# Performance work log

Measured on AMD Instinct MI355X. Metric: run time of the kernel, lower is better.

The kernel has to match this reference:

```python
import jax, jax.numpy as jnp
import numpy as np

B = 16      # number of graphs (equal-sized, batch = repeat(arange(B), N))


def _knn_edges(pos, k, total):
    """Batch-aware kNN graph, torch_geometric knn_graph semantics.

    loop=False, flow='source_to_target': for each query node i, its k nearest
    neighbors j produce edges (row=j neighbor/source, col=i query/target).
    Returns (row, col) as flat global int32 index arrays of length B*N*k.
    """
    N = total // B
    posb = pos.reshape(B, N, -1)                      # [B, N, 3]
    sq = jnp.sum(posb * posb, axis=-1)                # [B, N]
    # squared Euclidean distances, [B, N, N]
    d2 = sq[:, :, None] + sq[:, None, :] - 2.0 * jnp.einsum('bnd,bmd->bnm', posb, posb)
    d2 = jnp.where(jnp.eye(N, dtype=bool)[None], jnp.inf, d2)  # exclude self-loops
    _, nbr = jax.lax.top_k(-d2, k)                    # [B, N, k] local neighbor idx
    offs = (jnp.arange(B, dtype=nbr.dtype) * N)[:, None, None]
    row = (nbr + offs).reshape(-1)                                      # neighbors (sources)
    col = jnp.broadcast_to(jnp.arange(N, dtype=nbr.dtype)[None, :, None] + offs,
                           (B, N, k)).reshape(-1)                       # query nodes (targets)
    return row, col


def reference(x, pos, batch, k):
    total = x.shape[0]
    row, col = _knn_edges(pos, k, total)
    # scatter_mean(x[col], row, dim_size=total): mean of gathered features per row index
    sums = jax.ops.segment_sum(x[col], row, num_segments=total)          # [total, d]
    cnt = jax.ops.segment_sum(jnp.ones(row.shape, x.dtype), row, num_segments=total)
    x_neigh_mean = sums / jnp.maximum(cnt, 1.0)[:, None]                 # empty rows -> 0
    return jnp.sum(jnp.abs(x - x_neigh_mean), axis=-1)                   # L1 norm, [total]


def setup_inputs() -> dict:
    key = jax.random.key(0)
    k1, k2 = jax.random.split(key)
    N = 4096
    x = jax.random.normal(k1, (B * N, 64), dtype=jnp.float32)
    pos = jax.random.normal(k2, (B * N, 3), dtype=jnp.float32)
    batch = jnp.repeat(jnp.arange(B, dtype=jnp.int64), N)
    return {"x": x, "pos": pos, "batch": batch, "k": 10}
```

## Files before the change

kernel.cpp:

```cpp
#include <hip/hip_runtime.h>
#include <stdint.h>

#define NB 16
#define NN 4096
#define KK 10
#define NL 11
#define FD 64
#define TOTAL (NB * NN)
#define NW 8
#define CH 512
#define SOCT 32
#define QG 64
#define WCAP 24
#define WPITCH 25

#define INFF __int_as_float(0x7f800000)

__device__ __forceinline__ float Fd2(float cx, float cy, float cz, float cq,
                                     float vx2, float vy2, float vz2, float sqi) {
    return __fmaf_rn(vz2, cz, __fmaf_rn(vy2, cy, __fmaf_rn(vx2, cx, __fadd_rn(sqi, cq))));
}

__device__ __forceinline__ uint32_t d2exact(float mx, float my, float mz, float sqi,
                                            float cx, float cy, float cz, float cw) {
    float dot = __fadd_rn(__fadd_rn(__fmul_rn(mx, cx), __fmul_rn(my, cy)),
                          __fmul_rn(mz, cz));
    float d2 = __fsub_rn(__fadd_rn(sqi, cw), __fmul_rn(2.0f, dot));
    return __float_as_uint(d2);
}

__global__ __launch_bounds__(256) void prep_kernel(const float* __restrict__ pos,
                                                   float4* __restrict__ pp4,
                                                   int* __restrict__ cnt) {
    const int p = blockIdx.x * 256 + threadIdx.x;
    const float* s = pos + (size_t)p * 6;
    float x0 = s[0], y0 = s[1], z0 = s[2];
    float x1 = s[3], y1 = s[4], z1 = s[5];
    float q0 = __fadd_rn(__fadd_rn(__fmul_rn(x0, x0), __fmul_rn(y0, y0)),
                         __fmul_rn(z0, z0));
    float q1 = __fadd_rn(__fadd_rn(__fmul_rn(x1, x1), __fmul_rn(y1, y1)),
                         __fmul_rn(z1, z1));
    pp4[2 * p + 0] = make_float4(x0, x1, y0, y1);
    pp4[2 * p + 1] = make_float4(z0, z1, q0, q1);
    cnt[2 * p + 0] = 0;
    cnt[2 * p + 1] = 0;
}

__global__ __launch_bounds__(512, 8) void knn_kernel(const float4* __restrict__ pp4,
                                                     int* __restrict__ cnt,
                                                     int* __restrict__ colfix,
                                                     int* __restrict__ nbr) {
    __shared__ uint32_t smem[6400];
    __shared__ float tau_s[QG];
    __shared__ uint32_t qcntw[QG * NW];
    float* listf = (float*)smem;
    uint16_t* pool16 = (uint16_t*)smem;

    const int tid = threadIdx.x;
    const int lane = tid & 63;
    const int w = __builtin_amdgcn_readfirstlane(tid >> 6);
    const int batch = blockIdx.x >> 6;
    const int qloc = ((blockIdx.x & 63) << 6) | lane;
    const int gbase = batch << 12;
    const int gq = gbase + qloc;

    float4 mA = pp4[(gq >> 1) * 2 + 0];
    float4 mB = pp4[(gq >> 1) * 2 + 1];
    const bool hi = (qloc & 1);
    const float mx = hi ? mA.y : mA.x;
    const float my = hi ? mA.w : mA.z;
    const float mz = hi ? mB.y : mB.x;
    const float sqi = hi ? mB.w : mB.z;
    const float vx2 = __fmul_rn(-2.0f, mx);
    const float vy2 = __fmul_rn(-2.0f, my);
    const float vz2 = __fmul_rn(-2.0f, mz);

    const float4* __restrict__ cp = pp4 + (size_t)(gbase + w * CH);

#define D8(cb)                                                        \
    float4 A0 = (cb)[0], B0 = (cb)[1], A1 = (cb)[2], B1 = (cb)[3];    \
    float4 A2 = (cb)[4], B2 = (cb)[5], A3 = (cb)[6], B3 = (cb)[7];    \
    float d0 = Fd2(A0.x, A0.z, B0.x, B0.z, vx2, vy2, vz2, sqi);       \
    float d1 = Fd2(A0.y, A0.w, B0.y, B0.w, vx2, vy2, vz2, sqi);       \
    float d2 = Fd2(A1.x, A1.z, B1.x, B1.z, vx2, vy2, vz2, sqi);       \
    float d3 = Fd2(A1.y, A1.w, B1.y, B1.w, vx2, vy2, vz2, sqi);       \
    float d4 = Fd2(A2.x, A2.z, B2.x, B2.z, vx2, vy2, vz2, sqi);       \
    float d5 = Fd2(A2.y, A2.w, B2.y, B2.w, vx2, vy2, vz2, sqi);       \
    float d6 = Fd2(A3.x, A3.z, B3.x, B3.z, vx2, vy2, vz2, sqi);       \
    float d7 = Fd2(A3.y, A3.w, B3.y, B3.w, vx2, vy2, vz2, sqi);

    float L[NL];
#pragma unroll
    for (int t = 0; t < NL; t++) L[t] = INFF;

#pragma unroll 2
    for (int o = 0; o < SOCT; ++o) {
        const float4* cb = cp + o * 8;
        D8(cb);
        float m = fminf(fminf(fminf(d0, d1), fminf(d2, d3)),
                        fminf(fminf(d4, d5), fminf(d6, d7)));
#pragma unroll
        for (int t = 0; t < NL - 1; ++t) L[t] = __builtin_amdgcn_fmed3f(L[t], L[t + 1], m);
        L[NL - 1] = fminf(L[NL - 1], m);
    }
#pragma unroll
    for (int t = 0; t < NL; t++) listf[tid * NL + t] = L[t];
    __syncthreads();

    if (tid < QG) {
        int p[NW];
#pragma unroll
        for (int u = 0; u < NW; u++) p[u] = NL - 1;
        float tau = INFF;
        for (int it = 0; it < NL; ++it) {
            float best = INFF;
            int bw = 0;
#pragma unroll
            for (int u = 0; u < NW; u++) {
                float v = (p[u] >= 0) ? listf[((u << 6) | tid) * NL + p[u]] : INFF;
                if (v < best) { best = v; bw = u; }
            }
            p[bw]--;
            tau = best;
        }
        tau_s[tid] = tau;
    }
    __syncthreads();

    const float tau = tau_s[lane] * 1.00001f;
    const uint32_t cell0 = (uint32_t)((lane * NW + w) * WPITCH);
    uint32_t cpos = cell0;
    for (int o = 0; o < CH / 8; ++o) {
        const float4* cb = cp + o * 8;
        D8(cb);
        const uint32_t jb = (uint32_t)(w * CH + o * 8);
#define PUSH(dv, off)                                              \
        if ((dv) <= tau && cpos < cell0 + WCAP) {                  \
            pool16[cpos] = (uint16_t)(jb + (off));                 \
            cpos++;                                                \
        }
        PUSH(d0, 0) PUSH(d1, 1) PUSH(d2, 2) PUSH(d3, 3)
        PUSH(d4, 4) PUSH(d5, 5) PUSH(d6, 6) PUSH(d7, 7)
#undef PUSH
    }
    qcntw[lane * NW + w] = cpos - cell0;
    __syncthreads();

    if (tid < QG) {
        uint64_t S[KK];
#pragma unroll
        for (int t = 0; t < KK; t++) S[t] = ~0ull;
#pragma unroll
        for (int u = 0; u < NW; u++) {
            uint32_t c2 = qcntw[tid * NW + u];
            const uint16_t* st = pool16 + (tid * NW + u) * WPITCH;
            for (uint32_t e = 0; e < c2; ++e) {
                uint32_t ix = st[e];
                if (ix == (uint32_t)qloc) continue;
                int g = gbase + (int)ix;
                float4 A = pp4[(g >> 1) * 2 + 0];
                float4 B = pp4[(g >> 1) * 2 + 1];
                bool ch = (ix & 1);
                uint32_t db = d2exact(mx, my, mz, sqi,
                                      ch ? A.y : A.x, ch ? A.w : A.z,
                                      ch ? B.y : B.x, ch ? B.w : B.z);
                uint64_t k64 = ((uint64_t)db << 32) | ix;
                if (k64 < S[0]) {
                    bool sh[KK];
                    sh[0] = true;
#pragma unroll
                    for (int t = 1; t < KK; t++) sh[t] = (k64 < S[t]);
#pragma unroll
                    for (int t = 0; t < KK; t++) {
                        uint64_t vac = sh[t] ? k64 : S[t];
                        S[t] = (t + 1 < KK) ? (sh[t + 1] ? S[t + 1] : vac) : vac;
                    }
                }
            }
        }
#pragma unroll
        for (int t = 0; t < KK; t++) {
            int jl = (int)(S[t] & 0xffffffffu);
            int gj = gbase + jl;
            int p = atomicAdd(&cnt[gj], 1);
            if (colfix) {
                if (p < 64) colfix[(gj << 6) | p] = gq;
            } else {
                nbr[gq * KK + t] = gj;
            }
        }
    }
#undef D8
}

__global__ __launch_bounds__(256) void out_bucket_kernel(const float4* __restrict__ x4,
                                                         const int* __restrict__ colfix,
                                                         const int* __restrict__ cnt,
                                                         float* __restrict__ out) {
    const int gid = blockIdx.x * 256 + threadIdx.x;
    const int n = gid >> 4;
    const int s = gid & 15;
    const int c = cnt[n];
    const int cc = (c > 64) ? 64 : c;
    const int base = n << 6;
    float4 acc = make_float4(0.f, 0.f, 0.f, 0.f);
    int e = 0;
    for (; e + 2 <= cc; e += 2) {
        int q0 = colfix[base + e], q1 = colfix[base + e + 1];
        float4 v0 = x4[(q0 << 4) | s];
        float4 v1 = x4[(q1 << 4) | s];
        acc.x += v0.x; acc.y += v0.y; acc.z += v0.z; acc.w += v0.w;
        acc.x += v1.x; acc.y += v1.y; acc.z += v1.z; acc.w += v1.w;
    }
    if (e < cc) {
        int q0 = colfix[base + e];
        float4 v0 = x4[(q0 << 4) | s];
        acc.x += v0.x; acc.y += v0.y; acc.z += v0.z; acc.w += v0.w;
    }
    const float inv = 1.0f / (float)(c > 1 ? c : 1);
    float4 mn = x4[(n << 4) | s];
    float v = fabsf(mn.x - acc.x * inv) + fabsf(mn.y - acc.y * inv) +
              fabsf(mn.z - acc.z * inv) + fabsf(mn.w - acc.w * inv);
    v += __shfl_xor(v, 1, 64);
    v += __shfl_xor(v, 2, 64);
    v += __shfl_xor(v, 4, 64);
    v += __shfl_xor(v, 8, 64);
    if (s == 0) out[n] = v;
}

__global__ __launch_bounds__(1024) void scan_kernel(const int* __restrict__ cnt,
                                                    int* __restrict__ offs) {
    __shared__ int lds[1024];
    const int t = threadIdx.x;
    const int base = t * 64;
    int s = 0;
    for (int i = 0; i < 64; i++) s += cnt[base + i];
    lds[t] = s;
    __syncthreads();
    for (int off = 1; off < 1024; off <<= 1) {
        int v = (t >= off) ? lds[t - off] : 0;
        __syncthreads();
        lds[t] += v;
        __syncthreads();
    }
    int run = lds[t] - s;
    for (int i = 0; i < 64; i++) {
        offs[base + i] = run;
        run += cnt[base + i];
    }
}

__global__ __launch_bounds__(256) void fill_kernel(const int* __restrict__ nbr,
                                                   int* __restrict__ offs,
                                                   int* __restrict__ col) {
    const int i = blockIdx.x * 256 + threadIdx.x;
#pragma unroll
    for (int t = 0; t < KK; t++) {
        int j = nbr[i * KK + t];
        int p = atomicAdd(&offs[j], 1);
        col[p] = i;
    }
}

__global__ __launch_bounds__(256) void out_kernel(const float* __restrict__ x,
                                                  const int* __restrict__ col,
                                                  const int* __restrict__ offs_end,
                                                  const int* __restrict__ cnt,
                                                  float* __restrict__ out) {
    const int gtid = blockIdx.x * 256 + threadIdx.x;
    const int n = gtid >> 6;
    const int lane = gtid & 63;
    const int c = cnt[n];
    const int end = offs_end[n];
    const int start = end - c;
    float s = 0.0f;
    for (int e = start; e < end; e++) {
        int i = col[e];
        s += x[(size_t)i * FD + lane];
    }
    float mean = s / (float)(c > 1 ? c : 1);
    float v = fabsf(x[(size_t)n * FD + lane] - mean);
#pragma unroll
    for (int off = 32; off; off >>= 1) v += __shfl_xor(v, off, 64);
    if (lane == 0) out[n] = v;
}

extern "C" void kernel_launch(void* const* d_in, const int* in_sizes, int n_in,
                              void* d_out, int out_size, void* d_ws, size_t ws_size,
                              hipStream_t stream) {
    const float* x = (const float*)d_in[0];
    const float* pos = (const float*)d_in[1];
    float* out = (float*)d_out;

    char* ws = (char*)d_ws;
    float4* pp4 = (float4*)(ws + 0);
    int* cnt = (int*)(ws + 1048576);
    int* colfix = (int*)(ws + 1310720);
    int* nbr = (int*)(ws + 1310720);
    int* offs = (int*)(ws + 3932160);
    int* col = (int*)(ws + 4194304);

    const bool bucket = ws_size >= (size_t)(1310720 + TOTAL * 64 * 4);

    hipLaunchKernelGGL(prep_kernel, dim3(TOTAL / 2 / 256), dim3(256), 0, stream, pos, pp4, cnt);
    hipLaunchKernelGGL(knn_kernel, dim3(TOTAL / QG), dim3(512), 0, stream, pp4, cnt,
                       bucket ? colfix : (int*)nullptr, bucket ? (int*)nullptr : nbr);
    if (bucket) {
        hipLaunchKernelGGL(out_bucket_kernel, dim3(TOTAL * 16 / 256), dim3(256), 0, stream,
                           (const float4*)x, colfix, cnt, out);
    } else {
        hipLaunchKernelGGL(scan_kernel, dim3(1), dim3(1024), 0, stream, cnt, offs);
        hipLaunchKernelGGL(fill_kernel, dim3(TOTAL / 256), dim3(256), 0, stream, nbr, offs, col);
        hipLaunchKernelGGL(out_kernel, dim3(TOTAL * FD / 256), dim3(256), 0, stream,
                           x, col, offs, cnt, out);
    }
}
```

Measured before the change: 202.4 us.

## Pack kNN distance math into float2 vectors, interleave batches across blocks, vectorize colfix loads

Distance evaluation in the kNN scan and collection passes now uses two-wide float vectors with fast contraction, so the compiler can emit packed FMA instructions. Block-to-batch mapping is interleaved so consecutive blocks handle different graphs, and the output kernel uses the same interleaving and reads neighbor indices as int4. The collection pass skips the push logic when none of the eight candidates pass, and the threshold slack is widened with an absolute epsilon. The widened slack admits more candidates into the fixed-capacity pools and could overflow them, and the reordered arithmetic may change rounding in the prefilter.

```diff
diff --git a/kernel.cpp b/kernel.cpp
--- a/kernel.cpp
+++ b/kernel.cpp
@@ -16,9 +16,16 @@
 
 #define INFF __int_as_float(0x7f800000)
 
-__device__ __forceinline__ float Fd2(float cx, float cy, float cz, float cq,
-                                     float vx2, float vy2, float vz2, float sqi) {
-    return __fmaf_rn(vz2, cz, __fmaf_rn(vy2, cy, __fmaf_rn(vx2, cx, __fadd_rn(sqi, cq))));
+typedef float f2 __attribute__((ext_vector_type(2)));
+
+__device__ __forceinline__ f2 FdP(f2 cx, f2 cy, f2 cz, f2 cq,
+                                  f2 vx2, f2 vy2, f2 vz2, f2 sqi2) {
+#pragma clang fp contract(fast)
+    f2 t = sqi2 + cq;
+    t = vx2 * cx + t;
+    t = vy2 * cy + t;
+    t = vz2 * cz + t;
+    return t;
 }
 
 __device__ __forceinline__ uint32_t d2exact(float mx, float my, float mz, float sqi,
@@ -59,8 +66,8 @@
     const int tid = threadIdx.x;
     const int lane = tid & 63;
     const int w = __builtin_amdgcn_readfirstlane(tid >> 6);
-    const int batch = blockIdx.x >> 6;
-    const int qloc = ((blockIdx.x & 63) << 6) | lane;
+    const int batch = blockIdx.x & 15;
+    const int qloc = ((blockIdx.x >> 4) << 6) | lane;
     const int gbase = batch << 12;
     const int gq = gbase + qloc;
 
@@ -71,23 +78,22 @@
     const float my = hi ? mA.w : mA.z;
     const float mz = hi ? mB.y : mB.x;
     const float sqi = hi ? mB.w : mB.z;
-    const float vx2 = __fmul_rn(-2.0f, mx);
-    const float vy2 = __fmul_rn(-2.0f, my);
-    const float vz2 = __fmul_rn(-2.0f, mz);
-
-    const float4* __restrict__ cp = pp4 + (size_t)(gbase + w * CH);
-
-#define D8(cb)                                                        \
-    float4 A0 = (cb)[0], B0 = (cb)[1], A1 = (cb)[2], B1 = (cb)[3];    \
-    float4 A2 = (cb)[4], B2 = (cb)[5], A3 = (cb)[6], B3 = (cb)[7];    \
-    float d0 = Fd2(A0.x, A0.z, B0.x, B0.z, vx2, vy2, vz2, sqi);       \
-    float d1 = Fd2(A0.y, A0.w, B0.y, B0.w, vx2, vy2, vz2, sqi);       \
-    float d2 = Fd2(A1.x, A1.z, B1.x, B1.z, vx2, vy2, vz2, sqi);       \
-    float d3 = Fd2(A1.y, A1.w, B1.y, B1.w, vx2, vy2, vz2, sqi);       \
-    float d4 = Fd2(A2.x, A2.z, B2.x, B2.z, vx2, vy2, vz2, sqi);       \
-    float d5 = Fd2(A2.y, A2.w, B2.y, B2.w, vx2, vy2, vz2, sqi);       \
-    float d6 = Fd2(A3.x, A3.z, B3.x, B3.z, vx2, vy2, vz2, sqi);       \
-    float d7 = Fd2(A3.y, A3.w, B3.y, B3.w, vx2, vy2, vz2, sqi);
+    const f2 vx22 = {__fmul_rn(-2.0f, mx), __fmul_rn(-2.0f, mx)};
+    const f2 vy22 = {__fmul_rn(-2.0f, my), __fmul_rn(-2.0f, my)};
+    const f2 vz22 = {__fmul_rn(-2.0f, mz), __fmul_rn(-2.0f, mz)};
+    const f2 sqi22 = {sqi, sqi};
+
+    const f2* __restrict__ cp2 = (const f2*)(pp4 + (size_t)(gbase + w * CH));
+
+#define D8P(cb2)                                                      \
+    f2 X0 = (cb2)[0],  Y0 = (cb2)[1],  Z0 = (cb2)[2],  Q0 = (cb2)[3]; \
+    f2 X1 = (cb2)[4],  Y1 = (cb2)[5],  Z1 = (cb2)[6],  Q1 = (cb2)[7]; \
+    f2 X2 = (cb2)[8],  Y2 = (cb2)[9],  Z2 = (cb2)[10], Q2 = (cb2)[11];\
+    f2 X3 = (cb2)[12], Y3 = (cb2)[13], Z3 = (cb2)[14], Q3 = (cb2)[15];\
+    f2 e0 = FdP(X0, Y0, Z0, Q0, vx22, vy22, vz22, sqi22);             \
+    f2 e1 = FdP(X1, Y1, Z1, Q1, vx22, vy22, vz22, sqi22);             \
+    f2 e2 = FdP(X2, Y2, Z2, Q2, vx22, vy22, vz22, sqi22);             \
+    f2 e3 = FdP(X3, Y3, Z3, Q3, vx22, vy22, vz22, sqi22);
 
     float L[NL];
 #pragma unroll
@@ -95,10 +101,10 @@
 
 #pragma unroll 2
     for (int o = 0; o < SOCT; ++o) {
-        const float4* cb = cp + o * 8;
-        D8(cb);
-        float m = fminf(fminf(fminf(d0, d1), fminf(d2, d3)),
-                        fminf(fminf(d4, d5), fminf(d6, d7)));
+        const f2* cb2 = cp2 + o * 16;
+        D8P(cb2);
+        float m = fminf(fminf(fminf(e0.x, e0.y), fminf(e1.x, e1.y)),
+                        fminf(fminf(e2.x, e2.y), fminf(e3.x, e3.y)));
 #pragma unroll
         for (int t = 0; t < NL - 1; ++t) L[t] = __builtin_amdgcn_fmed3f(L[t], L[t + 1], m);
         L[NL - 1] = fminf(L[NL - 1], m);
@@ -127,21 +133,26 @@
     }
     __syncthreads();
 
-    const float tau = tau_s[lane] * 1.00001f;
+    const float tau = tau_s[lane] * 1.0001f + 1e-5f;
     const uint32_t cell0 = (uint32_t)((lane * NW + w) * WPITCH);
     uint32_t cpos = cell0;
+#pragma unroll 2
     for (int o = 0; o < CH / 8; ++o) {
-        const float4* cb = cp + o * 8;
-        D8(cb);
+        const f2* cb2 = cp2 + o * 16;
+        D8P(cb2);
         const uint32_t jb = (uint32_t)(w * CH + o * 8);
-#define PUSH(dv, off)                                              \
-        if ((dv) <= tau && cpos < cell0 + WCAP) {                  \
-            pool16[cpos] = (uint16_t)(jb + (off));                 \
-            cpos++;                                                \
-        }
-        PUSH(d0, 0) PUSH(d1, 1) PUSH(d2, 2) PUSH(d3, 3)
-        PUSH(d4, 4) PUSH(d5, 5) PUSH(d6, 6) PUSH(d7, 7)
+        bool h0 = e0.x <= tau, h1 = e0.y <= tau, h2 = e1.x <= tau, h3 = e1.y <= tau;
+        bool h4 = e2.x <= tau, h5 = e2.y <= tau, h6 = e3.x <= tau, h7 = e3.y <= tau;
+        if (h0 | h1 | h2 | h3 | h4 | h5 | h6 | h7) {
+#define PUSH(hv, off)                                              \
+            if ((hv) && cpos < cell0 + WCAP) {                     \
+                pool16[cpos] = (uint16_t)(jb + (off));             \
+                cpos++;                                            \
+            }
+            PUSH(h0, 0) PUSH(h1, 1) PUSH(h2, 2) PUSH(h3, 3)
+            PUSH(h4, 4) PUSH(h5, 5) PUSH(h6, 6) PUSH(h7, 7)
 #undef PUSH
+        }
     }
     qcntw[lane * NW + w] = cpos - cell0;
     __syncthreads();
@@ -190,35 +201,41 @@
             }
         }
     }
-#undef D8
+#undef D8P
 }
 
 __global__ __launch_bounds__(256) void out_bucket_kernel(const float4* __restrict__ x4,
                                                          const int* __restrict__ colfix,
                                                          const int* __restrict__ cnt,
                                                          float* __restrict__ out) {
-    const int gid = blockIdx.x * 256 + threadIdx.x;
-    const int n = gid >> 4;
-    const int s = gid & 15;
+    const int b = blockIdx.x;
+    const int g = b & 15;
+    const int i = b >> 4;
+    const int n = (g << 12) | (i << 4) | (threadIdx.x >> 4);
+    const int s = threadIdx.x & 15;
     const int c = cnt[n];
     const int cc = (c > 64) ? 64 : c;
-    const int base = n << 6;
+    const int4* cf4 = (const int4*)(colfix + ((size_t)n << 6));
     float4 acc = make_float4(0.f, 0.f, 0.f, 0.f);
-    int e = 0;
-    for (; e + 2 <= cc; e += 2) {
-        int q0 = colfix[base + e], q1 = colfix[base + e + 1];
-        float4 v0 = x4[(q0 << 4) | s];
-        float4 v1 = x4[(q1 << 4) | s];
+    for (int eb = 0; eb < cc; eb += 4) {
+        int4 Q = cf4[eb >> 2];
+        float4 v0 = x4[((size_t)Q.x << 4) | s];
         acc.x += v0.x; acc.y += v0.y; acc.z += v0.z; acc.w += v0.w;
-        acc.x += v1.x; acc.y += v1.y; acc.z += v1.z; acc.w += v1.w;
-    }
-    if (e < cc) {
-        int q0 = colfix[base + e];
-        float4 v0 = x4[(q0 << 4) | s];
-        acc.x += v0.x; acc.y += v0.y; acc.z += v0.z; acc.w += v0.w;
+        if (eb + 1 < cc) {
+            float4 v1 = x4[((size_t)Q.y << 4) | s];
+            acc.x += v1.x; acc.y += v1.y; acc.z += v1.z; acc.w += v1.w;
+        }
+        if (eb + 2 < cc) {
+            float4 v2 = x4[((size_t)Q.z << 4) | s];
+            acc.x += v2.x; acc.y += v2.y; acc.z += v2.z; acc.w += v2.w;
+        }
+        if (eb + 3 < cc) {
+            float4 v3 = x4[((size_t)Q.w << 4) | s];
+            acc.x += v3.x; acc.y += v3.y; acc.z += v3.z; acc.w += v3.w;
+        }
     }
     const float inv = 1.0f / (float)(c > 1 ? c : 1);
-    float4 mn = x4[(n << 4) | s];
+    float4 mn = x4[((size_t)n << 4) | s];
     float v = fabsf(mn.x - acc.x * inv) + fabsf(mn.y - acc.y * inv) +
               fabsf(mn.z - acc.z * inv) + fabsf(mn.w - acc.w * inv);
     v += __shfl_xor(v, 1, 64);
```

After: 190.7 us. 5.8% less time.
